# Kernel optimization log

Hardware: AMD Instinct MI355X
Metric: run time of the kernel (lower is better)

The kernel has to match this reference:

```python
import jax, jax.numpy as jnp
import numpy as np

N_EMBD = 1024
HEAD_SIZE = 64
BATCH = 4
T = 4096  # == block_size


def setup_inputs() -> dict:
    key = jax.random.key(0)
    kx, kq, kk, kv = jax.random.split(key, 4)
    x = jax.random.normal(kx, (BATCH, T, N_EMBD), dtype=jnp.float32)
    Wq = jax.random.normal(kq, (N_EMBD, HEAD_SIZE), dtype=jnp.float32) * 0.02
    Wk = jax.random.normal(kk, (N_EMBD, HEAD_SIZE), dtype=jnp.float32) * 0.02
    Wv = jax.random.normal(kv, (N_EMBD, HEAD_SIZE), dtype=jnp.float32) * 0.02
    return {"x": x, "Wq": Wq, "Wk": Wk, "Wv": Wv}


def reference(x, Wq, Wk, Wv):
    # x: [B, T, C]; projections: [B, T, H]
    B, Tlen, C = x.shape
    q = jnp.einsum('btc,ch->bth', x, Wq)
    k = jnp.einsum('btc,ch->bth', x, Wk)
    v = jnp.einsum('btc,ch->bth', x, Wv)
    # NOTE: original scales by C**-0.5 where C = n_embd (input channels), not head_size
    scale = jnp.asarray(C, x.dtype) ** -0.5
    wei = jnp.einsum('bth,bsh->bts', q, k) * scale  # [B, T, T]
    causal = jnp.tril(jnp.ones((Tlen, Tlen), dtype=bool))
    wei = jnp.where(causal, wei, -jnp.inf)
    wei = jax.nn.softmax(wei, axis=-1)
    # dropout p=0.0 -> identity
    out = jnp.einsum('bts,bsh->bth', wei, v)  # [B, T, H]
    return out
```

## Files before the change

### kernel.cpp

```cpp
#include <hip/hip_runtime.h>
#include <math.h>

#define T_SEQ 4096
#define NBATCH 4
#define NEMBD 1024
#define HS 64
#define BT (NBATCH * T_SEQ)

typedef float f32x4 __attribute__((ext_vector_type(4)));
typedef short s8v  __attribute__((ext_vector_type(8)));
typedef short s4v  __attribute__((ext_vector_type(4)));

__device__ __forceinline__ short f2b_rne(float f) {
    union { float f; unsigned u; } v; v.f = f;
    unsigned r = v.u + 0x7fffu + ((v.u >> 16) & 1u);
    return (short)(r >> 16);
}
__device__ __forceinline__ unsigned pk2(float lo, float hi) {
    return __builtin_amdgcn_perm(__float_as_uint(hi), __float_as_uint(lo), 0x07060302u);
}

__global__ __launch_bounds__(256) void xcast_kernel(
        const float* __restrict__ x, short* __restrict__ xb) {
    size_t i = ((size_t)blockIdx.x * 256 + threadIdx.x) * 16;
    float4 a = *(const float4*)(x + i);
    float4 b = *(const float4*)(x + i + 4);
    float4 c = *(const float4*)(x + i + 8);
    float4 d = *(const float4*)(x + i + 12);
    union { s8v v; unsigned u[4]; } v0, v1;
    v0.u[0] = pk2(a.x, a.y); v0.u[1] = pk2(a.z, a.w);
    v0.u[2] = pk2(b.x, b.y); v0.u[3] = pk2(b.z, b.w);
    v1.u[0] = pk2(c.x, c.y); v1.u[1] = pk2(c.z, c.w);
    v1.u[2] = pk2(d.x, d.y); v1.u[3] = pk2(d.z, d.w);
    *(s8v*)(xb + i) = v0.v;
    *(s8v*)(xb + i + 8) = v1.v;
}

__global__ __launch_bounds__(256) void xtouch_kernel(
        const float* __restrict__ x, float* __restrict__ sink) {
    const float4* p = (const float4*)x;
    float s = 0.f;
    #pragma unroll
    for (int it = 0; it < 8; it++) {
        float4 v = p[(size_t)blockIdx.x * 2048 + it * 256 + threadIdx.x];
        s += v.x + v.y + v.z + v.w;
    }
    if (s == 1.0e38f) sink[0] = s;
}

__global__ __launch_bounds__(256) void wtrans_kernel(
        const float* __restrict__ Wq, const float* __restrict__ Wk,
        const float* __restrict__ Wv, short* __restrict__ Wt) {
    int e = blockIdx.x * 256 + threadIdx.x;
    int col = e & 63, k = (e >> 6) & 1023, mat = e >> 16;
    const float* W = (mat == 0) ? Wq : ((mat == 1) ? Wk : Wv);
    float scale = (mat == 0) ? 0.0450842298f : 1.0f;
    Wt[(size_t)(mat * 64 + col) * 1024 + k] = f2b_rne(W[k * 64 + col] * scale);
}

template<bool SRC_BF16>
__global__ __launch_bounds__(512) void proj_kernel(
        const void* __restrict__ xsrc, const short* __restrict__ Wt,
        short* __restrict__ QKV) {
    __shared__ short xs[32 * 72];
    __shared__ short wsh[192 * 72];
    int tid = threadIdx.x;
    int w = tid >> 6, l = tid & 63, quad = l >> 4, c16 = l & 15;
    int rt = w >> 2, cg = w & 3;
    int row0 = blockIdx.x * 32;
    short* VpT = QKV + 2 * (size_t)BT * HS;

    const short* xb = (const short*)xsrc;
    const float* xf = (const float*)xsrc;
    int xrow_b = tid >> 3,  xc8 = (tid & 7) * 8;
    int xrow_f = tid >> 4,  xc4 = (tid & 15) * 4;

    s8v  wreg[3];
    s8v  xreg_b;
    float4 xreg_f;
    #pragma unroll
    for (int i = 0; i < 3; i++) {
        int c = tid + 512 * i;
        wreg[i] = *(const s8v*)(Wt + (size_t)(c >> 3) * 1024 + ((c & 7) * 8));
    }
    if (SRC_BF16) {
        if (tid < 256) xreg_b = *(const s8v*)(xb + (size_t)(row0 + xrow_b) * 1024 + xc8);
    } else {
        xreg_f = *(const float4*)(xf + (size_t)(row0 + xrow_f) * 1024 + xc4);
    }

    f32x4 acc[3] = {};
    for (int ko = 0; ko < NEMBD; ko += 64) {
        #pragma unroll
        for (int i = 0; i < 3; i++) {
            int c = tid + 512 * i;
            *(s8v*)(wsh + (c >> 3) * 72 + ((c & 7) * 8)) = wreg[i];
        }
        if (SRC_BF16) {
            if (tid < 256) *(s8v*)(xs + xrow_b * 72 + xc8) = xreg_b;
        } else {
            union { s4v v; unsigned u[2]; } pkv;
            pkv.u[0] = pk2(xreg_f.x, xreg_f.y);
            pkv.u[1] = pk2(xreg_f.z, xreg_f.w);
            *(s4v*)(xs + xrow_f * 72 + xc4) = pkv.v;
        }
        __syncthreads();
        {
            int kn = (ko + 64 < NEMBD) ? (ko + 64) : 0;
            #pragma unroll
            for (int i = 0; i < 3; i++) {
                int c = tid + 512 * i;
                wreg[i] = *(const s8v*)(Wt + (size_t)(c >> 3) * 1024 + kn + ((c & 7) * 8));
            }
            if (SRC_BF16) {
                if (tid < 256) xreg_b = *(const s8v*)(xb + (size_t)(row0 + xrow_b) * 1024 + kn + xc8);
            } else {
                xreg_f = *(const float4*)(xf + (size_t)(row0 + xrow_f) * 1024 + kn + xc4);
            }
        }
        #pragma unroll
        for (int ks = 0; ks < 2; ks++) {
            s8v a = *(const s8v*)(xs + (rt * 16 + c16) * 72 + ks * 32 + quad * 8);
            #pragma unroll
            for (int j = 0; j < 3; j++) {
                s8v b = *(const s8v*)(wsh + (cg * 48 + j * 16 + c16) * 72 + ks * 32 + quad * 8);
                acc[j] = __builtin_amdgcn_mfma_f32_16x16x32_bf16(a, b, acc[j], 0, 0, 0);
            }
        }
        __syncthreads();
    }
    #pragma unroll
    for (int j = 0; j < 3; j++) {
        int g = cg * 48 + j * 16 + c16;
        int mat = g >> 6, h = g & 63;
        if (mat < 2) {
            #pragma unroll
            for (int r = 0; r < 4; r++) {
                int row = row0 + rt * 16 + quad * 4 + r;
                QKV[(size_t)mat * BT * HS + (size_t)row * HS + h] = f2b_rne(acc[j][r]);
            }
        } else {
            int tg = row0 + rt * 16 + quad * 4;
            int b = tg >> 12, t = tg & 4095;
            size_t base = (((size_t)((b * 64 + (t >> 6)) * 64 + h)) << 6) + (t & 63);
            s4v pv;
            #pragma unroll
            for (int r = 0; r < 4; r++) pv[r] = f2b_rne(acc[j][r]);
            *(s4v*)(VpT + base) = pv;
        }
    }
}

__global__ __launch_bounds__(512, 4) void attn_kernel(
        const short* __restrict__ QKV, float* __restrict__ out) {
    __shared__ float smem[9216];
    short* Ps = (short*)smem;

    int tid = threadIdx.x;
    int w = tid >> 6, l = tid & 63, quad = l >> 4, c16 = l & 15;
    int bi = blockIdx.x;
    int b  = (bi & 7) >> 1;
    int r8 = bi >> 3;
    int p  = bi & 1;
    int jt = (r8 < 32) ? (127 - (2 * r8 + p)) : (2 * (r8 - 32) + p);
    int q0 = jt * 32;

    const short* Qp  = QKV;
    const short* Kp  = QKV + (size_t)BT * HS;
    const short* VpT = QKV + 2 * (size_t)BT * HS;
    size_t bT = (size_t)b * T_SEQ;

    s8v qf[2][2];
    #pragma unroll
    for (int qt = 0; qt < 2; qt++)
        #pragma unroll
        for (int h = 0; h < 2; h++)
            qf[qt][h] = *(const s8v*)(Qp + (bT + q0 + qt * 16 + c16) * HS + h * 32 + quad * 8);

    f32x4 o[2][4] = {};
    float lsum[2] = {0.f, 0.f};
    int nkt = (q0 >> 6) + 1;
    short* Pw[2] = { Ps + (w * 2) * 1152, Ps + (w * 2 + 1) * 1152 };
    const short* kbase = Kp + (bT + c16) * HS + quad * 8;
    const short* vbase = VpT + (((size_t)((b * 64) * 64 + c16)) << 6) + quad * 8;

    for (int kt = w; kt < nkt; kt += 8) {
        int kb = kt * 64;
        bool last = (kt == nkt - 1);

        s8v kf[4][2];
        #pragma unroll
        for (int nt = 0; nt < 4; nt++) {
            const short* kr = kbase + (size_t)(kb + nt * 16) * HS;
            kf[nt][0] = *(const s8v*)kr;
            kf[nt][1] = *(const s8v*)(kr + 32);
        }
        f32x4 st[2][4];
        #pragma unroll
        for (int nt = 0; nt < 4; nt++) {
            f32x4 z0 = {0.f, 0.f, 0.f, 0.f}, z1 = {0.f, 0.f, 0.f, 0.f};
            z0 = __builtin_amdgcn_mfma_f32_16x16x32_bf16(kf[nt][0], qf[0][0], z0, 0, 0, 0);
            z0 = __builtin_amdgcn_mfma_f32_16x16x32_bf16(kf[nt][1], qf[0][1], z0, 0, 0, 0);
            z1 = __builtin_amdgcn_mfma_f32_16x16x32_bf16(kf[nt][0], qf[1][0], z1, 0, 0, 0);
            z1 = __builtin_amdgcn_mfma_f32_16x16x32_bf16(kf[nt][1], qf[1][1], z1, 0, 0, 0);
            st[0][nt] = z0; st[1][nt] = z1;
        }
        s8v vf[4][2];
        #pragma unroll
        for (int nt = 0; nt < 4; nt++) {
            const short* vr = vbase + (((size_t)(kt * 64 + nt * 16)) << 6);
            vf[nt][0] = *(const s8v*)vr;
            vf[nt][1] = *(const s8v*)(vr + 32);
        }
        #pragma unroll
        for (int qt = 0; qt < 2; qt++) {
            int qrow = q0 + qt * 16 + c16;
            #pragma unroll
            for (int nt = 0; nt < 4; nt++) {
                float pr[4];
                #pragma unroll
                for (int rr = 0; rr < 4; rr++) {
                    float v = st[qt][nt][rr];
                    if (last && (kb + nt * 16 + quad * 4 + rr > qrow)) v = -30000.f;
                    pr[rr] = __builtin_amdgcn_exp2f(v);
                    lsum[qt] += pr[rr];
                }
                union { s4v v; unsigned u[2]; } pkv;
                pkv.u[0] = pk2(pr[0], pr[1]); pkv.u[1] = pk2(pr[2], pr[3]);
                *(s4v*)(Pw[qt] + c16 * 72 + nt * 16 + quad * 4) = pkv.v;
            }
        }
        s8v pa[2][2];
        #pragma unroll
        for (int qt = 0; qt < 2; qt++) {
            pa[qt][0] = *(const s8v*)(Pw[qt] + c16 * 72 + quad * 8);
            pa[qt][1] = *(const s8v*)(Pw[qt] + c16 * 72 + quad * 8 + 32);
        }
        #pragma unroll
        for (int nt = 0; nt < 4; nt++)
            #pragma unroll
            for (int qt = 0; qt < 2; qt++) {
                o[qt][nt] = __builtin_amdgcn_mfma_f32_16x16x32_bf16(pa[qt][0], vf[nt][0], o[qt][nt], 0, 0, 0);
                o[qt][nt] = __builtin_amdgcn_mfma_f32_16x16x32_bf16(pa[qt][1], vf[nt][1], o[qt][nt], 0, 0, 0);
            }
    }

    #pragma unroll
    for (int qt = 0; qt < 2; qt++) {
        lsum[qt] += __shfl_xor(lsum[qt], 16);
        lsum[qt] += __shfl_xor(lsum[qt], 32);
    }

    #pragma unroll
    for (int qt = 0; qt < 2; qt++) {
        __syncthreads();
        #pragma unroll
        for (int nt = 0; nt < 4; nt++)
            *(f32x4*)(smem + ((w * 4 + nt) * 64 + l) * 4) = o[qt][nt];
        if (l < 16) smem[8192 + w * 16 + l] = lsum[qt];
        __syncthreads();
        if (w < 4) {
            f32x4 os = {0.f, 0.f, 0.f, 0.f}, ls = {0.f, 0.f, 0.f, 0.f};
            #pragma unroll
            for (int s = 0; s < 8; s++) {
                os += *(const f32x4*)(smem + ((s * 4 + w) * 64 + l) * 4);
                ls += *(const f32x4*)(smem + 8192 + s * 16 + quad * 4);
            }
            #pragma unroll
            for (int rr = 0; rr < 4; rr++)
                out[(bT + q0 + qt * 16 + quad * 4 + rr) * HS + w * 16 + c16] = os[rr] / ls[rr];
        }
    }
}

extern "C" void kernel_launch(void* const* d_in, const int* in_sizes, int n_in,
                              void* d_out, int out_size, void* d_ws, size_t ws_size,
                              hipStream_t stream) {
    const float* x  = (const float*)d_in[0];
    const float* Wq = (const float*)d_in[1];
    const float* Wk = (const float*)d_in[2];
    const float* Wv = (const float*)d_in[3];
    float* out = (float*)d_out;

    short* QKV = (short*)d_ws;
    short* Wt  = QKV + (size_t)3 * BT * HS;
    short* xb  = Wt + (size_t)192 * 1024;
    size_t need = ((size_t)3 * BT * HS + (size_t)192 * 1024 + (size_t)BT * NEMBD) * 2;

    wtrans_kernel<<<768, 256, 0, stream>>>(Wq, Wk, Wv, Wt);
    if (ws_size >= need) {
        xcast_kernel<<<4096, 256, 0, stream>>>(x, xb);
        proj_kernel<true><<<BT / 32, 512, 0, stream>>>(xb, Wt, QKV);
    } else {
        xtouch_kernel<<<2048, 256, 0, stream>>>(x, (float*)d_ws);
        proj_kernel<false><<<BT / 32, 512, 0, stream>>>(x, Wt, QKV);
    }
    attn_kernel<<<512, 512, 0, stream>>>(QKV, out);
}
```

Baseline: 159.7 us.

## Split attention key range across two blocks and merge partials in a second kernel

Each 32-row query tile is now handled by two blocks, each covering half of the causal key range, so the attention grid doubles from 512 to 1024 blocks. Tiles are assigned in a serpentine order so per-block work is more even. Each block writes unnormalized partial outputs and row sums to workspace, and a new merge kernel adds the two halves and divides by the combined sum. MFMA sections are also wrapped in s_setprio to favor matrix issue. The cost is an extra launch and a round trip of partials through global memory.

```diff
diff --git a/kernel.cpp b/kernel.cpp
--- a/kernel.cpp
+++ b/kernel.cpp
@@ -152,7 +152,8 @@
 }
 
 __global__ __launch_bounds__(512, 4) void attn_kernel(
-        const short* __restrict__ QKV, float* __restrict__ out) {
+        const short* __restrict__ QKV, float* __restrict__ po,
+        float* __restrict__ pl) {
     __shared__ float smem[9216];
     short* Ps = (short*)smem;
 
@@ -160,10 +161,15 @@
     int w = tid >> 6, l = tid & 63, quad = l >> 4, c16 = l & 15;
     int bi = blockIdx.x;
     int b  = (bi & 7) >> 1;
-    int r8 = bi >> 3;
     int p  = bi & 1;
-    int jt = (r8 < 32) ? (127 - (2 * r8 + p)) : (2 * (r8 - 32) + p);
+    int r  = bi >> 3;
+    int k5 = r >> 5, m = r & 31;
+    int jt = k5 * 32 + ((k5 & 1) ? (31 - m) : m);
     int q0 = jt * 32;
+    int nkt = (q0 >> 6) + 1;
+    int mid = nkt >> 1;
+    int k0 = p ? mid : 0;
+    int k1 = p ? nkt : mid;
 
     const short* Qp  = QKV;
     const short* Kp  = QKV + (size_t)BT * HS;
@@ -179,12 +185,11 @@
 
     f32x4 o[2][4] = {};
     float lsum[2] = {0.f, 0.f};
-    int nkt = (q0 >> 6) + 1;
     short* Pw[2] = { Ps + (w * 2) * 1152, Ps + (w * 2 + 1) * 1152 };
     const short* kbase = Kp + (bT + c16) * HS + quad * 8;
     const short* vbase = VpT + (((size_t)((b * 64) * 64 + c16)) << 6) + quad * 8;
 
-    for (int kt = w; kt < nkt; kt += 8) {
+    for (int kt = k0 + w; kt < k1; kt += 8) {
         int kb = kt * 64;
         bool last = (kt == nkt - 1);
 
@@ -196,6 +201,7 @@
             kf[nt][1] = *(const s8v*)(kr + 32);
         }
         f32x4 st[2][4];
+        __builtin_amdgcn_s_setprio(1);
         #pragma unroll
         for (int nt = 0; nt < 4; nt++) {
             f32x4 z0 = {0.f, 0.f, 0.f, 0.f}, z1 = {0.f, 0.f, 0.f, 0.f};
@@ -205,6 +211,7 @@
             z1 = __builtin_amdgcn_mfma_f32_16x16x32_bf16(kf[nt][1], qf[1][1], z1, 0, 0, 0);
             st[0][nt] = z0; st[1][nt] = z1;
         }
+        __builtin_amdgcn_s_setprio(0);
         s8v vf[4][2];
         #pragma unroll
         for (int nt = 0; nt < 4; nt++) {
@@ -236,6 +243,7 @@
             pa[qt][0] = *(const s8v*)(Pw[qt] + c16 * 72 + quad * 8);
             pa[qt][1] = *(const s8v*)(Pw[qt] + c16 * 72 + quad * 8 + 32);
         }
+        __builtin_amdgcn_s_setprio(1);
         #pragma unroll
         for (int nt = 0; nt < 4; nt++)
             #pragma unroll
@@ -243,6 +251,7 @@
                 o[qt][nt] = __builtin_amdgcn_mfma_f32_16x16x32_bf16(pa[qt][0], vf[nt][0], o[qt][nt], 0, 0, 0);
                 o[qt][nt] = __builtin_amdgcn_mfma_f32_16x16x32_bf16(pa[qt][1], vf[nt][1], o[qt][nt], 0, 0, 0);
             }
+        __builtin_amdgcn_s_setprio(0);
     }
 
     #pragma unroll
@@ -266,11 +275,37 @@
                 os += *(const f32x4*)(smem + ((s * 4 + w) * 64 + l) * 4);
                 ls += *(const f32x4*)(smem + 8192 + s * 16 + quad * 4);
             }
+            float* pb = po + (size_t)bi * 2048 + qt * 1024;
             #pragma unroll
             for (int rr = 0; rr < 4; rr++)
-                out[(bT + q0 + qt * 16 + quad * 4 + rr) * HS + w * 16 + c16] = os[rr] / ls[rr];
-        }
-    }
+                pb[(quad * 4 + rr) * 64 + w * 16 + c16] = os[rr];
+            if (w == 0 && c16 == 0) {
+                #pragma unroll
+                for (int rr = 0; rr < 4; rr++)
+                    pl[bi * 32 + qt * 16 + quad * 4 + rr] = ls[rr];
+            }
+        }
+    }
+}
+
+__global__ __launch_bounds__(256) void merge_kernel(
+        const float* __restrict__ po, const float* __restrict__ pl,
+        float* __restrict__ out) {
+    int mb = blockIdx.x;
+    int b = mb >> 7, jt = mb & 127;
+    int k5 = jt >> 5, t = jt & 31;
+    int m = (k5 & 1) ? (31 - t) : t;
+    int bi0 = ((k5 * 32 + m) << 3) | (b << 1);
+    int e = threadIdx.x * 8;
+    int row = e >> 6;
+    const float* p0 = po + (size_t)bi0 * 2048 + e;
+    const float* p1 = po + (size_t)(bi0 + 1) * 2048 + e;
+    f32x4 a0 = *(const f32x4*)p0 + *(const f32x4*)p1;
+    f32x4 a1 = *(const f32x4*)(p0 + 4) + *(const f32x4*)(p1 + 4);
+    float inv = 1.0f / (pl[bi0 * 32 + row] + pl[(bi0 + 1) * 32 + row]);
+    float* ob = out + (size_t)mb * 2048 + e;
+    *(f32x4*)ob = a0 * inv;
+    *(f32x4*)(ob + 4) = a1 * inv;
 }
 
 extern "C" void kernel_launch(void* const* d_in, const int* in_sizes, int n_in,
@@ -284,8 +319,12 @@
 
     short* QKV = (short*)d_ws;
     short* Wt  = QKV + (size_t)3 * BT * HS;
-    short* xb  = Wt + (size_t)192 * 1024;
-    size_t need = ((size_t)3 * BT * HS + (size_t)192 * 1024 + (size_t)BT * NEMBD) * 2;
+    float* po  = (float*)(Wt + (size_t)192 * 1024);
+    float* pl  = po + (size_t)1024 * 2048;
+    short* xb  = (short*)(pl + 32 * 1024);
+    size_t need = ((size_t)3 * BT * HS + (size_t)192 * 1024) * 2
+                + ((size_t)1024 * 2048 + 32 * 1024) * 4
+                + (size_t)BT * NEMBD * 2;
 
     wtrans_kernel<<<768, 256, 0, stream>>>(Wq, Wk, Wv, Wt);
     if (ws_size >= need) {
@@ -295,5 +334,6 @@
         xtouch_kernel<<<2048, 256, 0, stream>>>(x, (float*)d_ws);
         proj_kernel<false><<<BT / 32, 512, 0, stream>>>(x, Wt, QKV);
     }
-    attn_kernel<<<512, 512, 0, stream>>>(QKV, out);
-}
+    attn_kernel<<<1024, 512, 0, stream>>>(QKV, po, pl);
+    merge_kernel<<<512, 256, 0, stream>>>(po, pl, out);
+}
```

New measurement: 181.0 us. 13.4% more time.

## Halve attention query tile to 16 rows, double grid, add MFMA priority hints

Applied to the files above, without the earlier changes.

Each attention block now handles 16 query rows instead of 32, so the grid grows from 512 to 1024 blocks and per-thread register and LDS use shrinks. The goal is more parallelism and better load balance across CUs for the causal workload, with a simpler single-tile epilogue. In exchange, every K/V tile is loaded twice as often and each wave issues fewer MFMAs per load. It also wraps the MFMA sections in s_setprio to favour matrix issue.

```diff
diff --git a/kernel.cpp b/kernel.cpp
--- a/kernel.cpp
+++ b/kernel.cpp
@@ -153,34 +153,32 @@
 
 __global__ __launch_bounds__(512, 4) void attn_kernel(
         const short* __restrict__ QKV, float* __restrict__ out) {
-    __shared__ float smem[9216];
+    __shared__ float smem[8448];
     short* Ps = (short*)smem;
 
     int tid = threadIdx.x;
     int w = tid >> 6, l = tid & 63, quad = l >> 4, c16 = l & 15;
     int bi = blockIdx.x;
     int b  = (bi & 7) >> 1;
+    int qh = bi & 1;
     int r8 = bi >> 3;
-    int p  = bi & 1;
-    int jt = (r8 < 32) ? (127 - (2 * r8 + p)) : (2 * (r8 - 32) + p);
-    int q0 = jt * 32;
+    int jt = (r8 < 64) ? (127 - r8) : (r8 - 64);
+    int q0 = jt * 32 + qh * 16;
 
     const short* Qp  = QKV;
     const short* Kp  = QKV + (size_t)BT * HS;
     const short* VpT = QKV + 2 * (size_t)BT * HS;
     size_t bT = (size_t)b * T_SEQ;
 
-    s8v qf[2][2];
-    #pragma unroll
-    for (int qt = 0; qt < 2; qt++)
-        #pragma unroll
-        for (int h = 0; h < 2; h++)
-            qf[qt][h] = *(const s8v*)(Qp + (bT + q0 + qt * 16 + c16) * HS + h * 32 + quad * 8);
-
-    f32x4 o[2][4] = {};
-    float lsum[2] = {0.f, 0.f};
-    int nkt = (q0 >> 6) + 1;
-    short* Pw[2] = { Ps + (w * 2) * 1152, Ps + (w * 2 + 1) * 1152 };
+    s8v qf[2];
+    #pragma unroll
+    for (int h = 0; h < 2; h++)
+        qf[h] = *(const s8v*)(Qp + (bT + q0 + c16) * HS + h * 32 + quad * 8);
+
+    f32x4 o[4] = {};
+    float lsA = 0.f, lsB = 0.f;
+    int nkt = (jt >> 1) + 1;
+    short* Pw = Ps + w * 1152;
     const short* kbase = Kp + (bT + c16) * HS + quad * 8;
     const short* vbase = VpT + (((size_t)((b * 64) * 64 + c16)) << 6) + quad * 8;
 
@@ -195,81 +193,73 @@
             kf[nt][0] = *(const s8v*)kr;
             kf[nt][1] = *(const s8v*)(kr + 32);
         }
-        f32x4 st[2][4];
-        #pragma unroll
-        for (int nt = 0; nt < 4; nt++) {
-            f32x4 z0 = {0.f, 0.f, 0.f, 0.f}, z1 = {0.f, 0.f, 0.f, 0.f};
-            z0 = __builtin_amdgcn_mfma_f32_16x16x32_bf16(kf[nt][0], qf[0][0], z0, 0, 0, 0);
-            z0 = __builtin_amdgcn_mfma_f32_16x16x32_bf16(kf[nt][1], qf[0][1], z0, 0, 0, 0);
-            z1 = __builtin_amdgcn_mfma_f32_16x16x32_bf16(kf[nt][0], qf[1][0], z1, 0, 0, 0);
-            z1 = __builtin_amdgcn_mfma_f32_16x16x32_bf16(kf[nt][1], qf[1][1], z1, 0, 0, 0);
-            st[0][nt] = z0; st[1][nt] = z1;
-        }
+        f32x4 st[4];
+        __builtin_amdgcn_s_setprio(1);
+        #pragma unroll
+        for (int nt = 0; nt < 4; nt++) {
+            f32x4 z = {0.f, 0.f, 0.f, 0.f};
+            z = __builtin_amdgcn_mfma_f32_16x16x32_bf16(kf[nt][0], qf[0], z, 0, 0, 0);
+            z = __builtin_amdgcn_mfma_f32_16x16x32_bf16(kf[nt][1], qf[1], z, 0, 0, 0);
+            st[nt] = z;
+        }
+        __builtin_amdgcn_s_setprio(0);
         s8v vf[4][2];
         #pragma unroll
         for (int nt = 0; nt < 4; nt++) {
-            const short* vr = vbase + (((size_t)(kt * 64 + nt * 16)) << 6);
+            const short* vr = vbase + (((size_t)(kb + nt * 16)) << 6);
             vf[nt][0] = *(const s8v*)vr;
             vf[nt][1] = *(const s8v*)(vr + 32);
         }
-        #pragma unroll
-        for (int qt = 0; qt < 2; qt++) {
-            int qrow = q0 + qt * 16 + c16;
+        {
+            int qrow = q0 + c16;
             #pragma unroll
             for (int nt = 0; nt < 4; nt++) {
                 float pr[4];
                 #pragma unroll
                 for (int rr = 0; rr < 4; rr++) {
-                    float v = st[qt][nt][rr];
+                    float v = st[nt][rr];
                     if (last && (kb + nt * 16 + quad * 4 + rr > qrow)) v = -30000.f;
                     pr[rr] = __builtin_amdgcn_exp2f(v);
-                    lsum[qt] += pr[rr];
                 }
+                lsA += pr[0] + pr[1];
+                lsB += pr[2] + pr[3];
                 union { s4v v; unsigned u[2]; } pkv;
                 pkv.u[0] = pk2(pr[0], pr[1]); pkv.u[1] = pk2(pr[2], pr[3]);
-                *(s4v*)(Pw[qt] + c16 * 72 + nt * 16 + quad * 4) = pkv.v;
-            }
-        }
-        s8v pa[2][2];
-        #pragma unroll
-        for (int qt = 0; qt < 2; qt++) {
-            pa[qt][0] = *(const s8v*)(Pw[qt] + c16 * 72 + quad * 8);
-            pa[qt][1] = *(const s8v*)(Pw[qt] + c16 * 72 + quad * 8 + 32);
-        }
-        #pragma unroll
-        for (int nt = 0; nt < 4; nt++)
-            #pragma unroll
-            for (int qt = 0; qt < 2; qt++) {
-                o[qt][nt] = __builtin_amdgcn_mfma_f32_16x16x32_bf16(pa[qt][0], vf[nt][0], o[qt][nt], 0, 0, 0);
-                o[qt][nt] = __builtin_amdgcn_mfma_f32_16x16x32_bf16(pa[qt][1], vf[nt][1], o[qt][nt], 0, 0, 0);
-            }
-    }
-
-    #pragma unroll
-    for (int qt = 0; qt < 2; qt++) {
-        lsum[qt] += __shfl_xor(lsum[qt], 16);
-        lsum[qt] += __shfl_xor(lsum[qt], 32);
-    }
-
-    #pragma unroll
-    for (int qt = 0; qt < 2; qt++) {
-        __syncthreads();
-        #pragma unroll
-        for (int nt = 0; nt < 4; nt++)
-            *(f32x4*)(smem + ((w * 4 + nt) * 64 + l) * 4) = o[qt][nt];
-        if (l < 16) smem[8192 + w * 16 + l] = lsum[qt];
-        __syncthreads();
-        if (w < 4) {
-            f32x4 os = {0.f, 0.f, 0.f, 0.f}, ls = {0.f, 0.f, 0.f, 0.f};
-            #pragma unroll
-            for (int s = 0; s < 8; s++) {
-                os += *(const f32x4*)(smem + ((s * 4 + w) * 64 + l) * 4);
-                ls += *(const f32x4*)(smem + 8192 + s * 16 + quad * 4);
-            }
-            #pragma unroll
-            for (int rr = 0; rr < 4; rr++)
-                out[(bT + q0 + qt * 16 + quad * 4 + rr) * HS + w * 16 + c16] = os[rr] / ls[rr];
-        }
+                *(s4v*)(Pw + c16 * 72 + nt * 16 + quad * 4) = pkv.v;
+            }
+        }
+        s8v pa[2];
+        pa[0] = *(const s8v*)(Pw + c16 * 72 + quad * 8);
+        pa[1] = *(const s8v*)(Pw + c16 * 72 + quad * 8 + 32);
+        __builtin_amdgcn_s_setprio(1);
+        #pragma unroll
+        for (int nt = 0; nt < 4; nt++) {
+            o[nt] = __builtin_amdgcn_mfma_f32_16x16x32_bf16(pa[0], vf[nt][0], o[nt], 0, 0, 0);
+            o[nt] = __builtin_amdgcn_mfma_f32_16x16x32_bf16(pa[1], vf[nt][1], o[nt], 0, 0, 0);
+        }
+        __builtin_amdgcn_s_setprio(0);
+    }
+
+    float lsum = lsA + lsB;
+    lsum += __shfl_xor(lsum, 16);
+    lsum += __shfl_xor(lsum, 32);
+
+    __syncthreads();
+    #pragma unroll
+    for (int nt = 0; nt < 4; nt++)
+        *(f32x4*)(smem + ((w * 4 + nt) * 64 + l) * 4) = o[nt];
+    if (l < 16) smem[8192 + w * 16 + l] = lsum;
+    __syncthreads();
+    if (w < 4) {
+        f32x4 os = {0.f, 0.f, 0.f, 0.f}, ls = {0.f, 0.f, 0.f, 0.f};
+        #pragma unroll
+        for (int s = 0; s < 8; s++) {
+            os += *(const f32x4*)(smem + ((s * 4 + w) * 64 + l) * 4);
+            ls += *(const f32x4*)(smem + 8192 + s * 16 + quad * 4);
+        }
+        #pragma unroll
+        for (int rr = 0; rr < 4; rr++)
+            out[(bT + q0 + quad * 4 + rr) * HS + w * 16 + c16] = os[rr] / ls[rr];
     }
 }
 
@@ -295,5 +285,5 @@
         xtouch_kernel<<<2048, 256, 0, stream>>>(x, (float*)d_ws);
         proj_kernel<false><<<BT / 32, 512, 0, stream>>>(x, Wt, QKV);
     }
-    attn_kernel<<<512, 512, 0, stream>>>(QKV, out);
-}
+    attn_kernel<<<1024, 512, 0, stream>>>(QKV, out);
+}
```

Measured after the change: 199.3 us. 24.8% more time.
